# Kernel tuning notes

Hardware: AMD Instinct MI355X
Metric: run time of the kernel (lower is better)

The kernel has to match this reference:

```python
import jax, jax.numpy as jnp
import numpy as np

N_LAYERS = 6
EPS = 1e-5


def _s4d_layer(u, log_dt, C_re, C_im, log_A_real, A_imag, D, out_w, out_b):
    # u: (B, H, L). Standard S4D: diagonal SSM kernel -> FFT conv -> D skip -> GELU -> 1x1 conv + GLU.
    B, H, L = u.shape
    dt = jnp.exp(log_dt)                                   # (H,)
    A = -jnp.exp(log_A_real) + 1j * A_imag                 # (H, N2) complex
    dtA = A * dt[:, None]                                  # (H, N2)
    C = (C_re + 1j * C_im) * (jnp.exp(dtA) - 1.0) / A      # (H, N2) ZOH-discretized C
    V = jnp.exp(dtA[:, :, None] * jnp.arange(L))           # (H, N2, L) Vandermonde exp(dtA * l)
    k = 2.0 * jnp.einsum('hn,hnl->hl', C, V).real          # (H, L) SSM convolution kernel
    # circular conv via length-2L FFT (equivalent to causal linear conv, then truncate)
    k_f = jnp.fft.rfft(k, n=2 * L)                         # (H, L+1)
    u_f = jnp.fft.rfft(u, n=2 * L)                         # (B, H, L+1)
    y = jnp.fft.irfft(u_f * k_f, n=2 * L)[..., :L]         # (B, H, L)
    y = y + u * D[:, None]                                 # skip connection
    y = jax.nn.gelu(y, approximate=False)                  # torch nn.GELU (exact erf)
    y = jnp.einsum('bhl,gh->bgl', y, out_w) + out_b[:, None]  # 1x1 Conv1d -> (B, 2H, L)
    a, b = jnp.split(y, 2, axis=1)                         # GLU over channel dim (dim=-2)
    return a * jax.nn.sigmoid(b)


def _batchnorm(x, gamma, beta):
    # BatchNorm1d over (B, H, L): per-channel stats across batch and length (training-mode forward)
    mean = x.mean(axis=(0, 2), keepdims=True)
    var = x.var(axis=(0, 2), keepdims=True)
    return (x - mean) * jax.lax.rsqrt(var + EPS) * gamma[None, :, None] + beta[None, :, None]


def setup_inputs() -> dict:
    B, L, D_IN, H, N2 = 8, 5000, 12, 256, 32
    key = jax.random.key(0)
    ks = jax.random.split(key, 8)
    x = jax.random.normal(ks[0], (B, L, D_IN), jnp.float32)
    pre_w = jax.random.normal(ks[1], (H, D_IN), jnp.float32) / np.float32(np.sqrt(D_IN))
    pre_b = jnp.zeros((H,), jnp.float32)
    # log_dt ~ Uniform(log 0.001, log 0.1) as in S4DKernel init
    log_dt = (jax.random.uniform(ks[2], (N_LAYERS, H), jnp.float32)
              * np.float32(np.log(0.1) - np.log(0.001)) + np.float32(np.log(0.001)))
    C_re = jax.random.normal(ks[3], (N_LAYERS, H, N2), jnp.float32)
    C_im = jax.random.normal(ks[4], (N_LAYERS, H, N2), jnp.float32)
    log_A_real = jnp.full((N_LAYERS, H, N2), np.float32(np.log(0.5)), jnp.float32)
    A_imag = jnp.broadcast_to(np.float32(np.pi) * jnp.arange(N2, dtype=jnp.float32),
                              (N_LAYERS, H, N2)) + jnp.zeros((N_LAYERS, H, N2), jnp.float32)
    D = jax.random.normal(ks[5], (N_LAYERS, H), jnp.float32)
    out_w = jax.random.normal(ks[6], (N_LAYERS, 2 * H, H), jnp.float32) / np.float32(np.sqrt(H))
    out_b = jnp.zeros((N_LAYERS, 2 * H), jnp.float32)
    bn_gamma = jnp.ones((3, H), jnp.float32)
    bn_beta = jnp.zeros((3, H), jnp.float32)
    return {"x": x, "pre_w": pre_w, "pre_b": pre_b, "log_dt": log_dt, "C_re": C_re,
            "C_im": C_im, "log_A_real": log_A_real, "A_imag": A_imag, "D": D,
            "out_w": out_w, "out_b": out_b, "bn_gamma": bn_gamma, "bn_beta": bn_beta}


def reference(x, pre_w, pre_b, log_dt, C_re, C_im, log_A_real, A_imag, D, out_w, out_b, bn_gamma, bn_beta):
    h = x @ pre_w.T + pre_b          # (B, L, H) pre-projection
    h = jnp.swapaxes(h, -1, -2)      # (B, H, L)
    bn_idx = 0
    for i in range(N_LAYERS):
        z = _s4d_layer(h, log_dt[i], C_re[i], C_im[i], log_A_real[i], A_imag[i],
                       D[i], out_w[i], out_b[i])
        h = z + h                     # residual (dropout is identity in eval/reference)
        if i % 2 == 0:                # BatchNorm1d on even layers only
            h = _batchnorm(h, bn_gamma[bn_idx], bn_beta[bn_idx])
            bn_idx += 1
    return jnp.swapaxes(h, -1, -2)   # (B, L, H)
```

## Files before the change

### kernel.cpp

```cpp
#include <hip/hip_runtime.h>
#include <hip/hip_bf16.h>
#include <math.h>

#define NB 8
#define LSEQ 5000
#define DIN 12
#define HCH 256
#define N2C 32
#define NLAY 6
#define G2C 512
#define TTC 64
#define NCH 79
#define LPAD 5120

typedef __attribute__((ext_vector_type(8))) short bf8v;
typedef __attribute__((ext_vector_type(8))) unsigned short us8v;
typedef __attribute__((ext_vector_type(4))) float f32x4;

#define MFMA16(a,b,c) __builtin_amdgcn_mfma_f32_16x16x32_bf16((a),(b),(c),0,0,0)

static __device__ __forceinline__ unsigned short f2bf(float f){
  unsigned int u = __float_as_uint(f);
  u = u + 0x7FFFu + ((u >> 16) & 1u);
  return (unsigned short)(u >> 16);
}
static __device__ __forceinline__ float bf2f(unsigned short s){
  return __uint_as_float(((unsigned int)s) << 16);
}
static __device__ __forceinline__ bf8v pack8(float4 a, float4 b){
  bf8v r;
  r[0]=(short)f2bf(a.x); r[1]=(short)f2bf(a.y); r[2]=(short)f2bf(a.z); r[3]=(short)f2bf(a.w);
  r[4]=(short)f2bf(b.x); r[5]=(short)f2bf(b.y); r[6]=(short)f2bf(b.z); r[7]=(short)f2bf(b.w);
  return r;
}
static __device__ __forceinline__ float gelu_f(float x){
  return 0.5f*x*(1.0f + erff(x*0.70710678118654752f));
}
static __device__ __forceinline__ float sigm(float x){
  return 1.0f/(1.0f + expf(-x));
}


__global__ __launch_bounds__(256) void kp_params(
    const float* __restrict__ log_dt, const float* __restrict__ lAr,
    const float* __restrict__ A_im, const float* __restrict__ C_re,
    const float* __restrict__ C_im,
    float* __restrict__ p_ar, float* __restrict__ p_ai,
    float* __restrict__ p_cer, float* __restrict__ p_cei,
    float* __restrict__ p_wtr, float* __restrict__ p_wti)
{
  int idx = blockIdx.x*256 + threadIdx.x;
  int lh = idx >> 5;
  float dt = expf(log_dt[lh]);
  float Are = -expf(lAr[idx]);
  float Aim = A_im[idx];
  float ar = Are*dt, ai = Aim*dt;
  float er = expf(ar);
  float wr = er*cosf(ai), wi = er*sinf(ai);
  float inv = 1.0f/(Are*Are + Aim*Aim);
  float tr = ((wr-1.0f)*Are + wi*Aim)*inv;
  float ti = (wi*Are - (wr-1.0f)*Aim)*inv;
  p_cer[idx] = C_re[idx]*tr - C_im[idx]*ti;
  p_cei[idx] = C_re[idx]*ti + C_im[idx]*tr;
  p_ar[idx] = ar; p_ai[idx] = ai;
  float eT = expf(ar*64.0f);
  p_wtr[idx] = eT*cosf(ai*64.0f);
  p_wti[idx] = eT*sinf(ai*64.0f);
}

__global__ __launch_bounds__(256) void kp_kk(
    const float* __restrict__ p_ar, const float* __restrict__ p_ai,
    const float* __restrict__ p_cer, const float* __restrict__ p_cei,
    float* __restrict__ kk)
{
  int idx = blockIdx.x*256 + threadIdx.x;
  int d = idx & 63, lh = idx >> 6;
  int base = lh*N2C;
  float fd = (float)d;
  float s = 0.0f;
  for (int n=0; n<N2C; n++){
    float ar = p_ar[base+n], ai = p_ai[base+n];
    float e = expf(ar*fd);
    float pr = e*cosf(ai*fd), pi = e*sinf(ai*fd);
    s += p_cer[base+n]*pr - p_cei[base+n]*pi;
  }
  kk[idx] = 2.0f*s;
}

__global__ __launch_bounds__(256) void kp_A2(
    const float* __restrict__ p_ar, const float* __restrict__ p_ai,
    const float* __restrict__ p_cer, const float* __restrict__ p_cei,
    const float* __restrict__ kk, unsigned short* __restrict__ A2b)
{
  int idx = blockIdx.x*256 + threadIdx.x;
  int kcol = idx & 127;
  int t = (idx >> 7) & 63;
  int lh = idx >> 13;
  float v;
  if (kcol < 64){
    v = (kcol <= t) ? kk[lh*64 + (t - kcol)] : 0.0f;
  } else {
    int q = kcol - 64, n = q >> 1;
    int p = lh*N2C + n;
    float fp = (float)(t+1);
    float e = expf(p_ar[p]*fp);
    float pr = e*cosf(p_ai[p]*fp), pi = e*sinf(p_ai[p]*fp);
    float cer = p_cer[p], cei = p_cei[p];
    v = (q&1) ? -2.0f*(cer*pi + cei*pr) : 2.0f*(cer*pr - cei*pi);
  }
  A2b[idx] = f2bf(v);
}

__global__ __launch_bounds__(256) void kp_Vm(
    const float* __restrict__ p_ar, const float* __restrict__ p_ai,
    unsigned short* __restrict__ Vmb)
{
  int idx = blockIdx.x*256 + threadIdx.x;
  int j = idx & 63;
  int q = (idx >> 6) & 63;
  int lh = idx >> 12;
  int n = q >> 1;
  int p = lh*N2C + n;
  float fp = (float)(63 - j);
  float e = expf(p_ar[p]*fp);
  float pr = e*cosf(p_ai[p]*fp), pi = e*sinf(p_ai[p]*fp);
  Vmb[idx] = f2bf((q&1) ? pi : pr);
}

__global__ __launch_bounds__(256) void kp_Wp(
    const float* __restrict__ out_w, const float* __restrict__ out_b,
    unsigned short* __restrict__ Wpb, float* __restrict__ bp)
{
  int idx = blockIdx.x*256 + threadIdx.x;
  int hcol = idx & 255;
  int g2 = (idx >> 8) & 511;
  int li = idx >> 17;
  int src = (g2 >> 1) + ((g2 & 1) ? HCH : 0);
  Wpb[idx] = f2bf(out_w[((size_t)li*G2C + src)*HCH + hcol]);
  if (hcol == 0) bp[li*G2C + g2] = out_b[li*G2C + src];
}


__global__ __launch_bounds__(256) void k_preproj(
    const float* __restrict__ x, const float* __restrict__ pre_w,
    const float* __restrict__ pre_b, float* __restrict__ hbuf)
{
  int l = blockIdx.x*256 + threadIdx.x;
  int hc = blockIdx.y, b = blockIdx.z;
  if (l >= LSEQ) return;
  const float* xr = x + (size_t)(b*LSEQ + l)*DIN;
  const float* wr = pre_w + hc*DIN;
  float acc = pre_b[hc];
  #pragma unroll
  for (int d=0; d<DIN; d++) acc += xr[d]*wr[d];
  hbuf[(size_t)(b*HCH + hc)*LSEQ + l] = acc;
}


template<int DO_BN>
__global__ __launch_bounds__(320, 4) void k_row(
    const unsigned short* __restrict__ Vm, const unsigned short* __restrict__ A2,
    const float* __restrict__ wtr, const float* __restrict__ wti,
    const float* __restrict__ Dg, float* __restrict__ hbuf,
    const float* __restrict__ scale, const float* __restrict__ shift,
    unsigned short* __restrict__ yg, int layer)
{
  __shared__ float su[5120];
  __shared__ float sE[5120];
  int id = blockIdx.x;
  int xcd = id & 7, local = id >> 3;
  int hc = xcd*32 + (local >> 3);
  int b  = local & 7;
  int bh = b*HCH + hc;
  int tid = threadIdx.x, wid = tid>>6, lane = tid&63;
  float* hrow = hbuf + (size_t)bh*LSEQ;
  float bsc = 1.0f, bsh = 0.0f;
  if (DO_BN){ bsc = scale[hc]; bsh = shift[hc]; }
  #pragma unroll
  for (int i=0;i<4;i++){
    int q = tid + i*320;
    float4 v = {0,0,0,0};
    if (q < 1250) v = *(const float4*)(hrow + q*4);
    if (DO_BN){
      v.x=v.x*bsc+bsh; v.y=v.y*bsc+bsh; v.z=v.z*bsc+bsh; v.w=v.w*bsc+bsh;
      if (q < 1250) *(float4*)(hrow + q*4) = v;
    }
    int p = q ^ (((q>>4)&7)<<1);
    *(float4*)(su + p*4) = v;
  }
  __syncthreads();

  int craw = wid*16 + (lane&15);
  int c = craw < NCH ? craw : NCH-1;
  int krow8 = (lane>>4)*8;
  int swz = (c&7)<<1;

  {
    const unsigned short* Vp = Vm + (size_t)(layer*HCH + hc)*TTC*TTC + (size_t)(lane&15)*TTC;
    f32x4 a0={0,0,0,0},a1={0,0,0,0},a2={0,0,0,0},a3={0,0,0,0};
    #pragma unroll
    for (int ks=0; ks<2; ks++){
      int kb = ks*32 + krow8;
      int p0 = (c*16 + (kb>>2)) ^ swz;
      float4 u0 = *(const float4*)(su + p0*4);
      float4 u1 = *(const float4*)(su + p0*4 + 4);
      bf8v bfr = pack8(u0,u1);
      a0 = MFMA16(*(const bf8v*)(Vp + 0*16*TTC + kb), bfr, a0);
      a1 = MFMA16(*(const bf8v*)(Vp + 1*16*TTC + kb), bfr, a1);
      a2 = MFMA16(*(const bf8v*)(Vp + 2*16*TTC + kb), bfr, a2);
      a3 = MFMA16(*(const bf8v*)(Vp + 3*16*TTC + kb), bfr, a3);
    }
    if (craw >= NCH){
      a0=(f32x4){0,0,0,0}; a1=(f32x4){0,0,0,0};
      a2=(f32x4){0,0,0,0}; a3=(f32x4){0,0,0,0};
    }
    int j0 = craw*16 + (lane>>4);
    int sw2 = (craw&7)<<1;
    *(f32x4*)(sE + (size_t)((j0+ 0)^sw2)*4) = a0;
    *(f32x4*)(sE + (size_t)((j0+ 4)^sw2)*4) = a1;
    *(f32x4*)(sE + (size_t)((j0+ 8)^sw2)*4) = a2;
    *(f32x4*)(sE + (size_t)((j0+12)^sw2)*4) = a3;
  }
  __syncthreads();

  if (tid < 256){
    int n = tid >> 3, g = tid & 7;
    float wr = wtr[(layer*HCH+hc)*N2C + n];
    float wi = wti[(layer*HCH+hc)*N2C + n];
    int c0 = g*10;
    float tr_=0.0f, ti_=0.0f;
    #pragma unroll
    for (int k=0;k<10;k++){
      int cc = c0 + k;
      int p = ((cc*16 + (n>>1)) ^ ((cc&7)<<1))*4 + (n&1)*2;
      float2 e = *(float2*)(sE + p);
      float nr = wr*tr_ - wi*ti_ + e.x;
      ti_ = wr*ti_ + wi*tr_ + e.y;
      tr_ = nr;
    }
    float a2r = wr*wr - wi*wi,      a2i = 2.0f*wr*wi;
    float a4r = a2r*a2r - a2i*a2i,  a4i = 2.0f*a2r*a2i;
    float a8r = a4r*a4r - a4i*a4i,  a8i = 2.0f*a4r*a4i;
    float Ar = a8r*a2r - a8i*a2i,   Ai = a8r*a2i + a8i*a2r;
    float Br = tr_, Bi = ti_;
    #pragma unroll
    for (int st=1; st<8; st<<=1){
      float Ar2 = __shfl_up(Ar, st), Ai2 = __shfl_up(Ai, st);
      float Br2 = __shfl_up(Br, st), Bi2 = __shfl_up(Bi, st);
      if (g >= st){
        float nAr = Ar*Ar2 - Ai*Ai2;
        float nAi = Ar*Ai2 + Ai*Ar2;
        float nBr = Ar*Br2 - Ai*Bi2 + Br;
        float nBi = Ar*Bi2 + Ai*Br2 + Bi;
        Ar=nAr; Ai=nAi; Br=nBr; Bi=nBi;
      }
    }
    float Pr = __shfl_up(Br, 1), Pi = __shfl_up(Bi, 1);
    if (g == 0){ Pr = 0.0f; Pi = 0.0f; }
    #pragma unroll
    for (int k=0;k<10;k++){
      int cc = c0 + k;
      int p = ((cc*16 + (n>>1)) ^ ((cc&7)<<1))*4 + (n&1)*2;
      float2 e = *(float2*)(sE + p);
      *(float2*)(sE + p) = make_float2(Pr, Pi);
      float nr = wr*Pr - wi*Pi + e.x;
      Pi = wr*Pi + wi*Pr + e.y;
      Pr = nr;
    }
  }
  __syncthreads();

  f32x4 acc0={0,0,0,0},acc1={0,0,0,0},acc2={0,0,0,0},acc3={0,0,0,0};
  {
    const unsigned short* Ap = A2 + (size_t)(layer*HCH + hc)*TTC*128 + (size_t)(lane&15)*128;
    #pragma unroll
    for (int ks=0; ks<2; ks++){
      int kb = ks*32 + krow8;
      int p0 = (c*16 + (kb>>2)) ^ swz;
      float4 u0 = *(const float4*)(su + p0*4);
      float4 u1 = *(const float4*)(su + p0*4 + 4);
      bf8v bfr = pack8(u0,u1);
      acc0 = MFMA16(*(const bf8v*)(Ap + 0*16*128 + kb), bfr, acc0);
      acc1 = MFMA16(*(const bf8v*)(Ap + 1*16*128 + kb), bfr, acc1);
      acc2 = MFMA16(*(const bf8v*)(Ap + 2*16*128 + kb), bfr, acc2);
      acc3 = MFMA16(*(const bf8v*)(Ap + 3*16*128 + kb), bfr, acc3);
    }
    #pragma unroll
    for (int ks=2; ks<4; ks++){
      int kb = ks*32 + krow8;
      int p0 = (c*16 + ((kb-64)>>2)) ^ swz;
      float4 s0 = *(const float4*)(sE + p0*4);
      float4 s1 = *(const float4*)(sE + p0*4 + 4);
      bf8v bhv = pack8(s0,s1);
      acc0 = MFMA16(*(const bf8v*)(Ap + 0*16*128 + kb), bhv, acc0);
      acc1 = MFMA16(*(const bf8v*)(Ap + 1*16*128 + kb), bhv, acc1);
      acc2 = MFMA16(*(const bf8v*)(Ap + 2*16*128 + kb), bhv, acc2);
      acc3 = MFMA16(*(const bf8v*)(Ap + 3*16*128 + kb), bhv, acc3);
      float4 r0, r1;
      r0.x = s0.x - bf2f(f2bf(s0.x)); r0.y = s0.y - bf2f(f2bf(s0.y));
      r0.z = s0.z - bf2f(f2bf(s0.z)); r0.w = s0.w - bf2f(f2bf(s0.w));
      r1.x = s1.x - bf2f(f2bf(s1.x)); r1.y = s1.y - bf2f(f2bf(s1.y));
      r1.z = s1.z - bf2f(f2bf(s1.z)); r1.w = s1.w - bf2f(f2bf(s1.w));
      bf8v blv = pack8(r0,r1);
      acc0 = MFMA16(*(const bf8v*)(Ap + 0*16*128 + kb), blv, acc0);
      acc1 = MFMA16(*(const bf8v*)(Ap + 1*16*128 + kb), blv, acc1);
      acc2 = MFMA16(*(const bf8v*)(Ap + 2*16*128 + kb), blv, acc2);
      acc3 = MFMA16(*(const bf8v*)(Ap + 3*16*128 + kb), blv, acc3);
    }
  }
  __syncthreads();

  {
    float* ybuf = sE;
    float Dv = Dg[layer*HCH + hc];
    int tq = (lane>>4)*4;
    int qb = craw*16 + (tq>>2);
    int sw2 = (craw&7)<<1;
    float4 u4, o4;
    u4 = *(const float4*)(su + (size_t)((qb+ 0)^sw2)*4);
    o4.x = gelu_f(acc0[0] + Dv*u4.x); o4.y = gelu_f(acc0[1] + Dv*u4.y);
    o4.z = gelu_f(acc0[2] + Dv*u4.z); o4.w = gelu_f(acc0[3] + Dv*u4.w);
    *(float4*)(ybuf + (size_t)((qb+ 0)^sw2)*4) = o4;
    u4 = *(const float4*)(su + (size_t)((qb+ 4)^sw2)*4);
    o4.x = gelu_f(acc1[0] + Dv*u4.x); o4.y = gelu_f(acc1[1] + Dv*u4.y);
    o4.z = gelu_f(acc1[2] + Dv*u4.z); o4.w = gelu_f(acc1[3] + Dv*u4.w);
    *(float4*)(ybuf + (size_t)((qb+ 4)^sw2)*4) = o4;
    u4 = *(const float4*)(su + (size_t)((qb+ 8)^sw2)*4);
    o4.x = gelu_f(acc2[0] + Dv*u4.x); o4.y = gelu_f(acc2[1] + Dv*u4.y);
    o4.z = gelu_f(acc2[2] + Dv*u4.z); o4.w = gelu_f(acc2[3] + Dv*u4.w);
    *(float4*)(ybuf + (size_t)((qb+ 8)^sw2)*4) = o4;
    u4 = *(const float4*)(su + (size_t)((qb+12)^sw2)*4);
    o4.x = gelu_f(acc3[0] + Dv*u4.x); o4.y = gelu_f(acc3[1] + Dv*u4.y);
    o4.z = gelu_f(acc3[2] + Dv*u4.z); o4.w = gelu_f(acc3[3] + Dv*u4.w);
    *(float4*)(ybuf + (size_t)((qb+12)^sw2)*4) = o4;
  }
  __syncthreads();
  unsigned short* ygp = yg + (size_t)bh*LSEQ;
  #pragma unroll
  for (int pass=0; pass<2; pass++){
    int l0 = (pass*320 + tid)*8;
    if (l0 < LSEQ){
      int q0 = l0 >> 2;
      int p0 = q0 ^ (((q0>>4)&7)<<1);
      int q1 = q0 + 1;
      int p1 = q1 ^ (((q1>>4)&7)<<1);
      float4 v0 = *(const float4*)(sE + (size_t)p0*4);
      float4 v1 = *(const float4*)(sE + (size_t)p1*4);
      us8v o;
      o[0]=f2bf(v0.x); o[1]=f2bf(v0.y); o[2]=f2bf(v0.z); o[3]=f2bf(v0.w);
      o[4]=f2bf(v1.x); o[5]=f2bf(v1.y); o[6]=f2bf(v1.z); o[7]=f2bf(v1.w);
      *(us8v*)(ygp + l0) = o;
    }
  }
}


__global__ __launch_bounds__(256) void k_T(
    const unsigned short* __restrict__ yg, unsigned short* __restrict__ ygT)
{
  __shared__ unsigned short tile[64][72];
  int b = blockIdx.z, h0 = blockIdx.y*64, l0 = blockIdx.x*64;
  int tid = threadIdx.x;
  #pragma unroll
  for (int i=0;i<2;i++){
    int lidx = tid + i*256;
    int row = lidx>>3, c8 = (lidx&7)*8;
    us8v v = 0;
    if (l0 + c8 < LSEQ)
      v = *(const us8v*)(yg + (size_t)(b*HCH + h0 + row)*LSEQ + l0 + c8);
    *(us8v*)(&tile[row][c8]) = v;
  }
  __syncthreads();
  #pragma unroll
  for (int i=0;i<2;i++){
    int widx = tid + i*256;
    int r = widx>>3, h8 = (widx&7)*8;
    int l = l0 + r;
    us8v o = 0;
    if (l < LSEQ){
      #pragma unroll
      for (int e=0;e<8;e++) o[e] = tile[h8+e][r];
    }
    *(us8v*)(ygT + ((size_t)b*LPAD + l)*HCH + h0 + h8) = o;
  }
}


static __device__ __forceinline__ void stageA(
    const unsigned short* __restrict__ g, unsigned short* sbuf, int tid)
{
  #pragma unroll
  for (int i=0;i<8;i++){
    int p = i*256 + tid;
    int row = p>>5, kc = p&31;
    int kcl = kc ^ (row&7);
    const unsigned short* ga = g + (size_t)row*HCH + kcl*8;
    __builtin_amdgcn_global_load_lds(
        (const __attribute__((address_space(1))) void*)ga,
        (__attribute__((address_space(3))) void*)(sbuf + p*8),
        16, 0, 0);
  }
}
static __device__ __forceinline__ void stageB(
    const unsigned short* __restrict__ g, unsigned short* sbuf, int tid)
{
  #pragma unroll
  for (int i=0;i<4;i++){
    int p = i*256 + tid;
    int row = p>>5, kc = p&31;
    int kcl = kc ^ (row&7);
    const unsigned short* ga = g + (size_t)row*HCH + kcl*8;
    __builtin_amdgcn_global_load_lds(
        (const __attribute__((address_space(1))) void*)ga,
        (__attribute__((address_space(3))) void*)(sbuf + p*8),
        16, 0, 0);
  }
}
static __device__ __forceinline__ bf8v ldsF(const unsigned short* sbuf, int row, int k0){
  int byte = (row<<9) + (k0<<1);
  byte ^= ((row&7)<<4);
  return *(const bf8v*)((const char*)sbuf + byte);
}

template<int DO_STATS>
__global__ __launch_bounds__(256, 2) void k_gemm(
    const unsigned short* __restrict__ Wp, const float* __restrict__ bp,
    const unsigned short* __restrict__ ygT, float* __restrict__ hbuf,
    float* __restrict__ bnsum, float* __restrict__ bnsq, int layer)
{
  __shared__ unsigned short As[64*256];
  __shared__ unsigned short Bs[3][32*256];
  int id = blockIdx.x;
  int x = id & 7, s = id >> 3;
  int gt = s & 7;
  int q = x*8 + (s>>3);
  int b = q >> 3, lg = q & 7;
  int l0 = lg*640;

  int tid = threadIdx.x, wid = tid>>6, lane = tid&63;
  int wm = wid>>1, wn = wid&1;
  int colA = lane&15, krow8 = (lane>>4)*8;

  const unsigned short* Wt = Wp + (size_t)layer*G2C*HCH + (size_t)(gt*64)*HCH;
  const unsigned short* Yb = ygT + (size_t)b*LPAD*HCH;

  stageA(Wt, As, tid);
  stageB(Yb + (size_t)l0*HCH,      Bs[0], tid);
  stageB(Yb + (size_t)(l0+32)*HCH, Bs[1], tid);

  float4 bias4[2]; int hc0[2];
  #pragma unroll
  for (int m=0;m<2;m++){
    int g2r4 = gt*64 + wm*32 + m*16 + (lane>>4)*4;
    bias4[m] = *(const float4*)(bp + layer*G2C + g2r4);
    hc0[m] = g2r4 >> 1;
  }
  float sacc[4], qacc[4];
  if (DO_STATS){
    #pragma unroll
    for (int i=0;i<4;i++){ sacc[i]=0.0f; qacc[i]=0.0f; }
  }

  const int NT = 20;
  for (int t=0; t<NT; t++){
    __builtin_amdgcn_s_barrier();
    if (t+2 < NT)
      stageB(Yb + (size_t)(l0 + (t+2)*32)*HCH, Bs[(t+2)%3], tid);
    if (t+2 < NT)      asm volatile("s_waitcnt vmcnt(8)" ::: "memory");
    else if (t+1 < NT) asm volatile("s_waitcnt vmcnt(4)" ::: "memory");
    else               asm volatile("s_waitcnt vmcnt(0)" ::: "memory");
    __builtin_amdgcn_s_barrier();
    const unsigned short* Bc = Bs[t%3];
    f32x4 acc0 = (f32x4){0,0,0,0}, acc1 = (f32x4){0,0,0,0};
    #pragma unroll
    for (int ks=0; ks<8; ks++){
      int k0 = ks*32 + krow8;
      bf8v fb  = ldsF(Bc, wn*16 + colA, k0);
      bf8v fa0 = ldsF(As, wm*32 + colA, k0);
      bf8v fa1 = ldsF(As, wm*32 + 16 + colA, k0);
      acc0 = MFMA16(fa0, fb, acc0);
      acc1 = MFMA16(fa1, fb, acc1);
    }
    int l = l0 + t*32 + wn*16 + colA;
    #pragma unroll
    for (int m=0;m<2;m++){
      f32x4 av = m ? acc1 : acc0;
      float a0 = av[0] + bias4[m].x;
      float g0 = av[1] + bias4[m].y;
      float a1 = av[2] + bias4[m].z;
      float g1 = av[3] + bias4[m].w;
      float z0 = a0 * sigm(g0);
      float z1 = a1 * sigm(g1);
      float r0 = 0.0f, r1 = 0.0f;
      if (l < LSEQ){
        float* pp0 = hbuf + ((size_t)(b*HCH + hc0[m]))*LSEQ + l;
        float* pp1 = pp0 + LSEQ;
        r0 = z0 + pp0[0]; pp0[0] = r0;
        r1 = z1 + pp1[0]; pp1[0] = r1;
      }
      if (DO_STATS){
        sacc[m*2+0] += r0; qacc[m*2+0] += r0*r0;
        sacc[m*2+1] += r1; qacc[m*2+1] += r1*r1;
      }
    }
  }

  if (DO_STATS){
    #pragma unroll
    for (int m=0;m<2;m++){
      #pragma unroll
      for (int zr=0; zr<2; zr++){
        float sv = sacc[m*2+zr], qv = qacc[m*2+zr];
        sv += __shfl_xor(sv,1); qv += __shfl_xor(qv,1);
        sv += __shfl_xor(sv,2); qv += __shfl_xor(qv,2);
        sv += __shfl_xor(sv,4); qv += __shfl_xor(qv,4);
        sv += __shfl_xor(sv,8); qv += __shfl_xor(qv,8);
        if ((lane&15)==0){
          atomicAdd(&bnsum[hc0[m]+zr], sv);
          atomicAdd(&bnsq[hc0[m]+zr], qv);
        }
      }
    }
  }
}


__global__ void k_bnfin(const float* __restrict__ bnsum, const float* __restrict__ bnsq,
    const float* __restrict__ gam, const float* __restrict__ bet,
    float* __restrict__ scale, float* __restrict__ shift, int bnidx)
{
  int hc = threadIdx.x;
  const float inv = 1.0f/40000.0f;
  float mean = bnsum[hc]*inv;
  float var = bnsq[hc]*inv - mean*mean;
  float sc = gam[bnidx*HCH + hc] * rsqrtf(var + 1e-5f);
  scale[hc] = sc;
  shift[hc] = bet[bnidx*HCH + hc] - mean*sc;
}


__global__ __launch_bounds__(256) void k_outT(const float* __restrict__ hbuf,
    float* __restrict__ out)
{
  __shared__ float tile[64][65];
  int b = blockIdx.z, h0 = blockIdx.y*64, l0 = blockIdx.x*64;
  int tid = threadIdx.x;
  #pragma unroll
  for (int i=0;i<4;i++){
    int lidx = tid + i*256;
    int row = lidx>>4, c4 = (lidx&15)*4;
    float4 v = {0,0,0,0};
    if (l0 + c4 < LSEQ)
      v = *(const float4*)(hbuf + (size_t)(b*HCH + h0 + row)*LSEQ + l0 + c4);
    tile[row][c4+0]=v.x; tile[row][c4+1]=v.y; tile[row][c4+2]=v.z; tile[row][c4+3]=v.w;
  }
  __syncthreads();
  #pragma unroll
  for (int i=0;i<4;i++){
    int widx = tid + i*256;
    int r = widx>>4, h4 = (widx&15)*4;
    int l = l0 + r;
    if (l < LSEQ){
      float4 o = { tile[h4+0][r], tile[h4+1][r], tile[h4+2][r], tile[h4+3][r] };
      *(float4*)(out + ((size_t)(b*LSEQ) + l)*HCH + h0 + h4) = o;
    }
  }
}


extern "C" void kernel_launch(void* const* d_in, const int* in_sizes, int n_in,
                              void* d_out, int out_size, void* d_ws, size_t ws_size,
                              hipStream_t stream)
{
  (void)in_sizes; (void)n_in; (void)out_size; (void)ws_size;
  const float* x      = (const float*)d_in[0];
  const float* pre_w  = (const float*)d_in[1];
  const float* pre_b  = (const float*)d_in[2];
  const float* log_dt = (const float*)d_in[3];
  const float* C_re   = (const float*)d_in[4];
  const float* C_im   = (const float*)d_in[5];
  const float* lAr    = (const float*)d_in[6];
  const float* A_im   = (const float*)d_in[7];
  const float* Dg     = (const float*)d_in[8];
  const float* out_w  = (const float*)d_in[9];
  const float* out_b  = (const float*)d_in[10];
  const float* gam    = (const float*)d_in[11];
  const float* bet    = (const float*)d_in[12];
  float* out = (float*)d_out;

  char* ws = (char*)d_ws;
  size_t off = 0;
  auto alloc = [&](size_t bytes)->char*{
    char* p = ws + off;
    off += (bytes + 255) & ~(size_t)255;
    return p;
  };
  float*          hbuf  = (float*)         alloc((size_t)(NB*HCH*LSEQ + 8192)*4);
  unsigned short* yg    = (unsigned short*)alloc((size_t)(NB*HCH*LSEQ + 64)*2);
  unsigned short* ygT   = (unsigned short*)alloc((size_t)NB*LPAD*HCH*2);
  float*          p_ar  = (float*)         alloc((size_t)NLAY*HCH*N2C*4);
  float*          p_ai  = (float*)         alloc((size_t)NLAY*HCH*N2C*4);
  float*          p_cer = (float*)         alloc((size_t)NLAY*HCH*N2C*4);
  float*          p_cei = (float*)         alloc((size_t)NLAY*HCH*N2C*4);
  float*          p_wtr = (float*)         alloc((size_t)NLAY*HCH*N2C*4);
  float*          p_wti = (float*)         alloc((size_t)NLAY*HCH*N2C*4);
  float*          kk    = (float*)         alloc((size_t)NLAY*HCH*TTC*4);
  unsigned short* A2b   = (unsigned short*)alloc((size_t)NLAY*HCH*TTC*128*2);
  unsigned short* Vmb   = (unsigned short*)alloc((size_t)NLAY*HCH*TTC*TTC*2);
  unsigned short* Wpb   = (unsigned short*)alloc((size_t)NLAY*G2C*HCH*2);
  float*          bp    = (float*)         alloc((size_t)NLAY*G2C*4);
  float*          bnst  = (float*)         alloc((size_t)4*HCH*4);
  float* bnsum = bnst, *bnsq = bnst + HCH, *bnscale = bnst + 2*HCH, *bnshift = bnst + 3*HCH;

  kp_params<<<(NLAY*HCH*N2C)/256, 256, 0, stream>>>(log_dt, lAr, A_im, C_re, C_im,
      p_ar, p_ai, p_cer, p_cei, p_wtr, p_wti);
  kp_kk<<<(NLAY*HCH*TTC)/256, 256, 0, stream>>>(p_ar, p_ai, p_cer, p_cei, kk);
  kp_A2<<<(NLAY*HCH*TTC*128)/256, 256, 0, stream>>>(p_ar, p_ai, p_cer, p_cei, kk, A2b);
  kp_Vm<<<(NLAY*HCH*TTC*TTC)/256, 256, 0, stream>>>(p_ar, p_ai, Vmb);
  kp_Wp<<<(NLAY*G2C*HCH)/256, 256, 0, stream>>>(out_w, out_b, Wpb, bp);

  k_preproj<<<dim3(20, HCH, NB), 256, 0, stream>>>(x, pre_w, pre_b, hbuf);

  for (int layer=0; layer<NLAY; layer++){
    if (layer & 1)
      k_row<1><<<NB*HCH, 320, 0, stream>>>(Vmb, A2b, p_wtr, p_wti, Dg, hbuf,
                                           bnscale, bnshift, yg, layer);
    else
      k_row<0><<<NB*HCH, 320, 0, stream>>>(Vmb, A2b, p_wtr, p_wti, Dg, hbuf,
                                           bnscale, bnshift, yg, layer);
    k_T<<<dim3(LPAD/64, HCH/64, NB), 256, 0, stream>>>(yg, ygT);
    if ((layer & 1) == 0){
      hipMemsetAsync(bnsum, 0, 2*HCH*sizeof(float), stream);
      k_gemm<1><<<512, 256, 0, stream>>>(Wpb, bp, ygT, hbuf, bnsum, bnsq, layer);
      k_bnfin<<<1, HCH, 0, stream>>>(bnsum, bnsq, gam, bet, bnscale, bnshift, layer/2);
    } else {
      k_gemm<0><<<512, 256, 0, stream>>>(Wpb, bp, ygT, hbuf, bnsum, bnsq, layer);
    }
  }
  k_outT<<<dim3(79, HCH/64, NB), 256, 0, stream>>>(hbuf, out);
}
```

Measured before the change: 850.5 us.

## Drop the transpose kernel, load untransposed activations in GEMM, store bf16 row staging

```diff
diff --git a/kernel.cpp b/kernel.cpp
--- a/kernel.cpp
+++ b/kernel.cpp
@@ -11,10 +11,10 @@
 #define G2C 512
 #define TTC 64
 #define NCH 79
-#define LPAD 5120
 
 typedef __attribute__((ext_vector_type(8))) short bf8v;
 typedef __attribute__((ext_vector_type(8))) unsigned short us8v;
+typedef __attribute__((ext_vector_type(4))) unsigned short us4v;
 typedef __attribute__((ext_vector_type(4))) float f32x4;
 
 #define MFMA16(a,b,c) __builtin_amdgcn_mfma_f32_16x16x32_bf16((a),(b),(c),0,0,0)
@@ -161,11 +161,11 @@
 __global__ __launch_bounds__(320, 4) void k_row(
     const unsigned short* __restrict__ Vm, const unsigned short* __restrict__ A2,
     const float* __restrict__ wtr, const float* __restrict__ wti,
-    const float* __restrict__ Dg, float* __restrict__ hbuf,
+    const float* __restrict__ Dg, const float* __restrict__ hbuf,
     const float* __restrict__ scale, const float* __restrict__ shift,
     unsigned short* __restrict__ yg, int layer)
 {
-  __shared__ float su[5120];
+  __shared__ unsigned short suh[5120];
   __shared__ float sE[5120];
   int id = blockIdx.x;
   int xcd = id & 7, local = id >> 3;
@@ -173,27 +173,30 @@
   int b  = local & 7;
   int bh = b*HCH + hc;
   int tid = threadIdx.x, wid = tid>>6, lane = tid&63;
-  float* hrow = hbuf + (size_t)bh*LSEQ;
+  const float* hrow = hbuf + (size_t)bh*LSEQ;
   float bsc = 1.0f, bsh = 0.0f;
   if (DO_BN){ bsc = scale[hc]; bsh = shift[hc]; }
   #pragma unroll
   for (int i=0;i<4;i++){
-    int q = tid + i*320;
+    int idx = tid + i*320;
     float4 v = {0,0,0,0};
-    if (q < 1250) v = *(const float4*)(hrow + q*4);
+    if (idx < 1250) v = *(const float4*)(hrow + idx*4);
     if (DO_BN){
-      v.x=v.x*bsc+bsh; v.y=v.y*bsc+bsh; v.z=v.z*bsc+bsh; v.w=v.w*bsc+bsh;
-      if (q < 1250) *(float4*)(hrow + q*4) = v;
-    }
-    int p = q ^ (((q>>4)&7)<<1);
-    *(float4*)(su + p*4) = v;
+      v.x=fmaf(v.x,bsc,bsh); v.y=fmaf(v.y,bsc,bsh);
+      v.z=fmaf(v.z,bsc,bsh); v.w=fmaf(v.w,bsc,bsh);
+    }
+    us4v pk;
+    pk[0]=f2bf(v.x); pk[1]=f2bf(v.y); pk[2]=f2bf(v.z); pk[3]=f2bf(v.w);
+    int q2 = idx>>1;
+    int pq = q2 ^ ((q2>>3)&7);
+    *(us4v*)(suh + pq*8 + (idx&1)*4) = pk;
   }
   __syncthreads();
 
   int craw = wid*16 + (lane&15);
   int c = craw < NCH ? craw : NCH-1;
   int krow8 = (lane>>4)*8;
-  int swz = (c&7)<<1;
+  int swz = c&7;
 
   {
     const unsigned short* Vp = Vm + (size_t)(layer*HCH + hc)*TTC*TTC + (size_t)(lane&15)*TTC;
@@ -201,10 +204,7 @@
     #pragma unroll
     for (int ks=0; ks<2; ks++){
       int kb = ks*32 + krow8;
-      int p0 = (c*16 + (kb>>2)) ^ swz;
-      float4 u0 = *(const float4*)(su + p0*4);
-      float4 u1 = *(const float4*)(su + p0*4 + 4);
-      bf8v bfr = pack8(u0,u1);
+      bf8v bfr = *(const bf8v*)(suh + (size_t)((c*8 + (kb>>3)) ^ swz)*8);
       a0 = MFMA16(*(const bf8v*)(Vp + 0*16*TTC + kb), bfr, a0);
       a1 = MFMA16(*(const bf8v*)(Vp + 1*16*TTC + kb), bfr, a1);
       a2 = MFMA16(*(const bf8v*)(Vp + 2*16*TTC + kb), bfr, a2);
@@ -215,7 +215,7 @@
       a2=(f32x4){0,0,0,0}; a3=(f32x4){0,0,0,0};
     }
     int j0 = craw*16 + (lane>>4);
-    int sw2 = (craw&7)<<1;
+    int sw2 = craw&7;
     *(f32x4*)(sE + (size_t)((j0+ 0)^sw2)*4) = a0;
     *(f32x4*)(sE + (size_t)((j0+ 4)^sw2)*4) = a1;
     *(f32x4*)(sE + (size_t)((j0+ 8)^sw2)*4) = a2;
@@ -232,7 +232,7 @@
     #pragma unroll
     for (int k=0;k<10;k++){
       int cc = c0 + k;
-      int p = ((cc*16 + (n>>1)) ^ ((cc&7)<<1))*4 + (n&1)*2;
+      int p = ((cc*16 + (n>>1)) ^ (cc&7))*4 + (n&1)*2;
       float2 e = *(float2*)(sE + p);
       float nr = wr*tr_ - wi*ti_ + e.x;
       ti_ = wr*ti_ + wi*tr_ + e.y;
@@ -260,7 +260,7 @@
     #pragma unroll
     for (int k=0;k<10;k++){
       int cc = c0 + k;
-      int p = ((cc*16 + (n>>1)) ^ ((cc&7)<<1))*4 + (n&1)*2;
+      int p = ((cc*16 + (n>>1)) ^ (cc&7))*4 + (n&1)*2;
       float2 e = *(float2*)(sE + p);
       *(float2*)(sE + p) = make_float2(Pr, Pi);
       float nr = wr*Pr - wi*Pi + e.x;
@@ -276,10 +276,7 @@
     #pragma unroll
     for (int ks=0; ks<2; ks++){
       int kb = ks*32 + krow8;
-      int p0 = (c*16 + (kb>>2)) ^ swz;
-      float4 u0 = *(const float4*)(su + p0*4);
-      float4 u1 = *(const float4*)(su + p0*4 + 4);
-      bf8v bfr = pack8(u0,u1);
+      bf8v bfr = *(const bf8v*)(suh + (size_t)((c*8 + (kb>>3)) ^ swz)*8);
       acc0 = MFMA16(*(const bf8v*)(Ap + 0*16*128 + kb), bfr, acc0);
       acc1 = MFMA16(*(const bf8v*)(Ap + 1*16*128 + kb), bfr, acc1);
       acc2 = MFMA16(*(const bf8v*)(Ap + 2*16*128 + kb), bfr, acc2);
@@ -288,9 +285,9 @@
     #pragma unroll
     for (int ks=2; ks<4; ks++){
       int kb = ks*32 + krow8;
-      int p0 = (c*16 + ((kb-64)>>2)) ^ swz;
-      float4 s0 = *(const float4*)(sE + p0*4);
-      float4 s1 = *(const float4*)(sE + p0*4 + 4);
+      int w = (kb-64)>>2;
+      float4 s0 = *(const float4*)(sE + (size_t)((c*16 + w  ) ^ swz)*4);
+      float4 s1 = *(const float4*)(sE + (size_t)((c*16 + w+1) ^ swz)*4);
       bf8v bhv = pack8(s0,s1);
       acc0 = MFMA16(*(const bf8v*)(Ap + 0*16*128 + kb), bhv, acc0);
       acc1 = MFMA16(*(const bf8v*)(Ap + 1*16*128 + kb), bhv, acc1);
@@ -314,74 +311,33 @@
     float* ybuf = sE;
     float Dv = Dg[layer*HCH + hc];
     int tq = (lane>>4)*4;
-    int qb = craw*16 + (tq>>2);
-    int sw2 = (craw&7)<<1;
-    float4 u4, o4;
-    u4 = *(const float4*)(su + (size_t)((qb+ 0)^sw2)*4);
-    o4.x = gelu_f(acc0[0] + Dv*u4.x); o4.y = gelu_f(acc0[1] + Dv*u4.y);
-    o4.z = gelu_f(acc0[2] + Dv*u4.z); o4.w = gelu_f(acc0[3] + Dv*u4.w);
-    *(float4*)(ybuf + (size_t)((qb+ 0)^sw2)*4) = o4;
-    u4 = *(const float4*)(su + (size_t)((qb+ 4)^sw2)*4);
-    o4.x = gelu_f(acc1[0] + Dv*u4.x); o4.y = gelu_f(acc1[1] + Dv*u4.y);
-    o4.z = gelu_f(acc1[2] + Dv*u4.z); o4.w = gelu_f(acc1[3] + Dv*u4.w);
-    *(float4*)(ybuf + (size_t)((qb+ 4)^sw2)*4) = o4;
-    u4 = *(const float4*)(su + (size_t)((qb+ 8)^sw2)*4);
-    o4.x = gelu_f(acc2[0] + Dv*u4.x); o4.y = gelu_f(acc2[1] + Dv*u4.y);
-    o4.z = gelu_f(acc2[2] + Dv*u4.z); o4.w = gelu_f(acc2[3] + Dv*u4.w);
-    *(float4*)(ybuf + (size_t)((qb+ 8)^sw2)*4) = o4;
-    u4 = *(const float4*)(su + (size_t)((qb+12)^sw2)*4);
-    o4.x = gelu_f(acc3[0] + Dv*u4.x); o4.y = gelu_f(acc3[1] + Dv*u4.y);
-    o4.z = gelu_f(acc3[2] + Dv*u4.z); o4.w = gelu_f(acc3[3] + Dv*u4.w);
-    *(float4*)(ybuf + (size_t)((qb+12)^sw2)*4) = o4;
+    int sw2 = craw&7;
+    #pragma unroll
+    for (int m=0;m<4;m++){
+      f32x4 av = (m==0)?acc0:((m==1)?acc1:((m==2)?acc2:acc3));
+      int base = m*16 + tq;
+      int pc_ = (craw*8 + (base>>3)) ^ sw2;
+      us4v uv = *(const us4v*)(suh + (size_t)pc_*8 + ((base>>2)&1)*4);
+      float4 o4;
+      o4.x = gelu_f(av[0] + Dv*bf2f(uv[0]));
+      o4.y = gelu_f(av[1] + Dv*bf2f(uv[1]));
+      o4.z = gelu_f(av[2] + Dv*bf2f(uv[2]));
+      o4.w = gelu_f(av[3] + Dv*bf2f(uv[3]));
+      int q4 = craw*16 + (base>>2);
+      *(float4*)(ybuf + (size_t)(q4 ^ sw2)*4) = o4;
+    }
   }
   __syncthreads();
   unsigned short* ygp = yg + (size_t)bh*LSEQ;
   #pragma unroll
-  for (int pass=0; pass<2; pass++){
-    int l0 = (pass*320 + tid)*8;
-    if (l0 < LSEQ){
-      int q0 = l0 >> 2;
-      int p0 = q0 ^ (((q0>>4)&7)<<1);
-      int q1 = q0 + 1;
-      int p1 = q1 ^ (((q1>>4)&7)<<1);
-      float4 v0 = *(const float4*)(sE + (size_t)p0*4);
-      float4 v1 = *(const float4*)(sE + (size_t)p1*4);
-      us8v o;
-      o[0]=f2bf(v0.x); o[1]=f2bf(v0.y); o[2]=f2bf(v0.z); o[3]=f2bf(v0.w);
-      o[4]=f2bf(v1.x); o[5]=f2bf(v1.y); o[6]=f2bf(v1.z); o[7]=f2bf(v1.w);
-      *(us8v*)(ygp + l0) = o;
-    }
-  }
-}
-
-
-__global__ __launch_bounds__(256) void k_T(
-    const unsigned short* __restrict__ yg, unsigned short* __restrict__ ygT)
-{
-  __shared__ unsigned short tile[64][72];
-  int b = blockIdx.z, h0 = blockIdx.y*64, l0 = blockIdx.x*64;
-  int tid = threadIdx.x;
-  #pragma unroll
-  for (int i=0;i<2;i++){
-    int lidx = tid + i*256;
-    int row = lidx>>3, c8 = (lidx&7)*8;
-    us8v v = 0;
-    if (l0 + c8 < LSEQ)
-      v = *(const us8v*)(yg + (size_t)(b*HCH + h0 + row)*LSEQ + l0 + c8);
-    *(us8v*)(&tile[row][c8]) = v;
-  }
-  __syncthreads();
-  #pragma unroll
-  for (int i=0;i<2;i++){
-    int widx = tid + i*256;
-    int r = widx>>3, h8 = (widx&7)*8;
-    int l = l0 + r;
-    us8v o = 0;
-    if (l < LSEQ){
-      #pragma unroll
-      for (int e=0;e<8;e++) o[e] = tile[h8+e][r];
-    }
-    *(us8v*)(ygT + ((size_t)b*LPAD + l)*HCH + h0 + h8) = o;
+  for (int pass=0; pass<4; pass++){
+    int idx = pass*320 + tid;
+    if (idx < 1250){
+      float4 v = *(const float4*)(sE + (size_t)(idx ^ ((idx>>4)&7))*4);
+      us4v o;
+      o[0]=f2bf(v.x); o[1]=f2bf(v.y); o[2]=f2bf(v.z); o[3]=f2bf(v.w);
+      *(us4v*)(ygp + idx*4) = o;
+    }
   }
 }
 
@@ -401,35 +357,22 @@
         16, 0, 0);
   }
 }
-static __device__ __forceinline__ void stageB(
-    const unsigned short* __restrict__ g, unsigned short* sbuf, int tid)
-{
-  #pragma unroll
-  for (int i=0;i<4;i++){
-    int p = i*256 + tid;
-    int row = p>>5, kc = p&31;
-    int kcl = kc ^ (row&7);
-    const unsigned short* ga = g + (size_t)row*HCH + kcl*8;
-    __builtin_amdgcn_global_load_lds(
-        (const __attribute__((address_space(1))) void*)ga,
-        (__attribute__((address_space(3))) void*)(sbuf + p*8),
-        16, 0, 0);
-  }
-}
 static __device__ __forceinline__ bf8v ldsF(const unsigned short* sbuf, int row, int k0){
   int byte = (row<<9) + (k0<<1);
   byte ^= ((row&7)<<4);
   return *(const bf8v*)((const char*)sbuf + byte);
 }
 
-template<int DO_STATS>
+template<int DO_STATS, int DO_BN>
 __global__ __launch_bounds__(256, 2) void k_gemm(
     const unsigned short* __restrict__ Wp, const float* __restrict__ bp,
-    const unsigned short* __restrict__ ygT, float* __restrict__ hbuf,
-    float* __restrict__ bnsum, float* __restrict__ bnsq, int layer)
+    const unsigned short* __restrict__ yg, float* __restrict__ hbuf,
+    float* __restrict__ bnsum, float* __restrict__ bnsq,
+    const float* __restrict__ scale, const float* __restrict__ shift,
+    float* __restrict__ dump, int layer)
 {
   __shared__ unsigned short As[64*256];
-  __shared__ unsigned short Bs[3][32*256];
+  __shared__ unsigned short Bs[2][32*256];
   int id = blockIdx.x;
   int x = id & 7, s = id >> 3;
   int gt = s & 7;
@@ -439,21 +382,24 @@
 
   int tid = threadIdx.x, wid = tid>>6, lane = tid&63;
   int wm = wid>>1, wn = wid&1;
-  int colA = lane&15, krow8 = (lane>>4)*8;
+  int colA = lane&15;
+  int krow8 = (lane>>4)*8;
 
   const unsigned short* Wt = Wp + (size_t)layer*G2C*HCH + (size_t)(gt*64)*HCH;
-  const unsigned short* Yb = ygT + (size_t)b*LPAD*HCH;
-
+  const unsigned short* Yh = yg + (size_t)(b*HCH + tid)*LSEQ + l0;
   stageA(Wt, As, tid);
-  stageB(Yb + (size_t)l0*HCH,      Bs[0], tid);
-  stageB(Yb + (size_t)(l0+32)*HCH, Bs[1], tid);
 
   float4 bias4[2]; int hc0[2];
+  float bsc0[2], bsh0[2], bsc1[2], bsh1[2];
   #pragma unroll
   for (int m=0;m<2;m++){
     int g2r4 = gt*64 + wm*32 + m*16 + (lane>>4)*4;
     bias4[m] = *(const float4*)(bp + layer*G2C + g2r4);
     hc0[m] = g2r4 >> 1;
+    if (DO_BN){
+      bsc0[m] = scale[hc0[m]];   bsh0[m] = shift[hc0[m]];
+      bsc1[m] = scale[hc0[m]+1]; bsh1[m] = shift[hc0[m]+1];
+    }
   }
   float sacc[4], qacc[4];
   if (DO_STATS){
@@ -461,16 +407,38 @@
     for (int i=0;i<4;i++){ sacc[i]=0.0f; qacc[i]=0.0f; }
   }
 
+  us8v R0[4], R1[4], R2[4], R3[4];
+  #define LOADSET(R, tt) { _Pragma("unroll") \
+    for (int i_=0;i_<4;i_++) R[i_] = *(const us8v*)(Yh + (size_t)(tt)*32 + i_*8); }
+  #define DSWR(R) { _Pragma("unroll") \
+    for (int i_=0;i_<4;i_++){ _Pragma("unroll") \
+      for (int e_=0;e_<8;e_++){ int row_ = i_*8+e_; \
+        int byte_ = row_*512 + ((tid*2) ^ ((row_&7)<<4)); \
+        *(unsigned short*)((char*)Bw + byte_) = R[i_][e_]; } } }
+
+  LOADSET(R0, 0); LOADSET(R1, 1);
+
   const int NT = 20;
+  #pragma unroll 4
   for (int t=0; t<NT; t++){
+    if (t==0)           asm volatile("s_waitcnt vmcnt(4)"  ::: "memory");
+    else if (t < NT-1)  asm volatile("s_waitcnt vmcnt(12)" ::: "memory");
+    else                asm volatile("s_waitcnt vmcnt(8)"  ::: "memory");
     __builtin_amdgcn_s_barrier();
-    if (t+2 < NT)
-      stageB(Yb + (size_t)(l0 + (t+2)*32)*HCH, Bs[(t+2)%3], tid);
-    if (t+2 < NT)      asm volatile("s_waitcnt vmcnt(8)" ::: "memory");
-    else if (t+1 < NT) asm volatile("s_waitcnt vmcnt(4)" ::: "memory");
-    else               asm volatile("s_waitcnt vmcnt(0)" ::: "memory");
+    unsigned short* Bw = Bs[t&1];
+    if ((t&3)==0)      DSWR(R0)
+    else if ((t&3)==1) DSWR(R1)
+    else if ((t&3)==2) DSWR(R2)
+    else               DSWR(R3);
+    if (t+2 < NT){
+      if (((t+2)&3)==0)      LOADSET(R0, t+2)
+      else if (((t+2)&3)==1) LOADSET(R1, t+2)
+      else if (((t+2)&3)==2) LOADSET(R2, t+2)
+      else                   LOADSET(R3, t+2);
+    }
+    asm volatile("s_waitcnt lgkmcnt(0)" ::: "memory");
     __builtin_amdgcn_s_barrier();
-    const unsigned short* Bc = Bs[t%3];
+    const unsigned short* Bc = Bs[t&1];
     f32x4 acc0 = (f32x4){0,0,0,0}, acc1 = (f32x4){0,0,0,0};
     #pragma unroll
     for (int ks=0; ks<8; ks++){
@@ -482,6 +450,8 @@
       acc1 = MFMA16(fa1, fb, acc1);
     }
     int l = l0 + t*32 + wn*16 + colA;
+    bool valid = (l < LSEQ);
+    float vmsk = valid ? 1.0f : 0.0f;
     #pragma unroll
     for (int m=0;m<2;m++){
       f32x4 av = m ? acc1 : acc0;
@@ -491,19 +461,25 @@
       float g1 = av[3] + bias4[m].w;
       float z0 = a0 * sigm(g0);
       float z1 = a1 * sigm(g1);
-      float r0 = 0.0f, r1 = 0.0f;
-      if (l < LSEQ){
-        float* pp0 = hbuf + ((size_t)(b*HCH + hc0[m]))*LSEQ + l;
-        float* pp1 = pp0 + LSEQ;
-        r0 = z0 + pp0[0]; pp0[0] = r0;
-        r1 = z1 + pp1[0]; pp1[0] = r1;
+      float* pp0 = hbuf + ((size_t)(b*HCH + hc0[m]))*LSEQ + l;
+      float* pp1 = pp0 + LSEQ;
+      if (!valid){ pp0 = dump + tid; pp1 = dump + 256 + tid; }
+      float o0 = pp0[0], o1 = pp1[0];
+      if (DO_BN){
+        o0 = fmaf(o0, bsc0[m], bsh0[m]);
+        o1 = fmaf(o1, bsc1[m], bsh1[m]);
       }
+      float r0 = z0 + o0, r1 = z1 + o1;
+      pp0[0] = r0; pp1[0] = r1;
       if (DO_STATS){
-        sacc[m*2+0] += r0; qacc[m*2+0] += r0*r0;
-        sacc[m*2+1] += r1; qacc[m*2+1] += r1*r1;
+        float s0 = r0*vmsk, s1 = r1*vmsk;
+        sacc[m*2+0] += s0; qacc[m*2+0] += s0*s0;
+        sacc[m*2+1] += s1; qacc[m*2+1] += s1*s1;
       }
     }
   }
+  #undef LOADSET
+  #undef DSWR
 
   if (DO_STATS){
     #pragma unroll
@@ -596,8 +572,7 @@
     return p;
   };
   float*          hbuf  = (float*)         alloc((size_t)(NB*HCH*LSEQ + 8192)*4);
-  unsigned short* yg    = (unsigned short*)alloc((size_t)(NB*HCH*LSEQ + 64)*2);
-  unsigned short* ygT   = (unsigned short*)alloc((size_t)NB*LPAD*HCH*2);
+  unsigned short* yg    = (unsigned short*)alloc((size_t)(NB*HCH*LSEQ + 8192)*2);
   float*          p_ar  = (float*)         alloc((size_t)NLAY*HCH*N2C*4);
   float*          p_ai  = (float*)         alloc((size_t)NLAY*HCH*N2C*4);
   float*          p_cer = (float*)         alloc((size_t)NLAY*HCH*N2C*4);
@@ -611,6 +586,7 @@
   float*          bp    = (float*)         alloc((size_t)NLAY*G2C*4);
   float*          bnst  = (float*)         alloc((size_t)4*HCH*4);
   float* bnsum = bnst, *bnsq = bnst + HCH, *bnscale = bnst + 2*HCH, *bnshift = bnst + 3*HCH;
+  float* dump = hbuf + (size_t)NB*HCH*LSEQ;
 
   kp_params<<<(NLAY*HCH*N2C)/256, 256, 0, stream>>>(log_dt, lAr, A_im, C_re, C_im,
       p_ar, p_ai, p_cer, p_cei, p_wtr, p_wti);
@@ -628,13 +604,14 @@
     else
       k_row<0><<<NB*HCH, 320, 0, stream>>>(Vmb, A2b, p_wtr, p_wti, Dg, hbuf,
                                            bnscale, bnshift, yg, layer);
-    k_T<<<dim3(LPAD/64, HCH/64, NB), 256, 0, stream>>>(yg, ygT);
     if ((layer & 1) == 0){
       hipMemsetAsync(bnsum, 0, 2*HCH*sizeof(float), stream);
-      k_gemm<1><<<512, 256, 0, stream>>>(Wpb, bp, ygT, hbuf, bnsum, bnsq, layer);
+      k_gemm<1,0><<<512, 256, 0, stream>>>(Wpb, bp, yg, hbuf, bnsum, bnsq,
+                                           bnscale, bnshift, dump, layer);
       k_bnfin<<<1, HCH, 0, stream>>>(bnsum, bnsq, gam, bet, bnscale, bnshift, layer/2);
     } else {
-      k_gemm<0><<<512, 256, 0, stream>>>(Wpb, bp, ygT, hbuf, bnsum, bnsq, layer);
+      k_gemm<0,1><<<512, 256, 0, stream>>>(Wpb, bp, yg, hbuf, bnsum, bnsq,
+                                           bnscale, bnshift, dump, layer);
     }
   }
   k_outT<<<dim3(79, HCH/64, NB), 256, 0, stream>>>(hbuf, out);
```

Measured after the change: 805.7 us. -5.3%, faster.
